# Performance work log

Hardware: AMD Instinct MI355X
Metric: run time of the kernel (lower is better)

## Reference

```python
import jax, jax.numpy as jnp
import numpy as np

B, NW, D, K = 16384, 32, 64, 512  # batch, n_windows, embedding_dim, codebook_size


def setup_inputs() -> dict:
    key = jax.random.key(0)
    k1, k2 = jax.random.split(key)
    ze = jax.random.normal(k1, (B, NW * D), dtype=jnp.float32)
    codebook = jax.random.normal(k2, (K, D), dtype=jnp.float32)
    return {"ze": ze, "codebook": codebook}


def reference(ze, codebook):
    # window-based VQ: split last dim into NW windows of size D, quantize each
    zew = ze.reshape(B, NW, D)
    # squared distances: ||ze||^2 + ||e||^2 - 2 ze.e^T  -> [B, NW, K]
    sq_norm = (
        jnp.sum(zew * zew, axis=-1, keepdims=True)
        + jnp.sum(codebook * codebook, axis=-1)
        - 2.0 * jnp.einsum("bwd,kd->bwk", zew, codebook)
    )
    indices = jnp.argmin(sq_norm, axis=-1)  # [B, NW]
    zq = codebook[indices].reshape(ze.shape)  # gather + concat over windows

    vq_e_loss = jnp.mean((zq - jax.lax.stop_gradient(ze)) ** 2)
    vq_commit_loss = jnp.mean((jax.lax.stop_gradient(zq) - ze) ** 2)

    # entropy term: counts of each code usage divided by 10 (as in original)
    counts = jnp.bincount(indices.reshape(-1), length=K)
    probs = counts.astype(jnp.float32) / 10.0
    entropy = jnp.sum(probs * jnp.log(probs + 1e-10))
    return indices, zq, vq_e_loss, vq_commit_loss, entropy
```

## Files before the change

### kernel.cpp

```cpp
#include <hip/hip_runtime.h>
#include <math.h>

#define DIM 64
#define KCB 512
#define NWIN 524288
#define ZQN (NWIN * DIM)
#define WPT 512
#define NBLK (NWIN / WPT)

typedef __attribute__((ext_vector_type(8))) short bf16x8;
typedef __attribute__((ext_vector_type(4))) float f32x4;

__device__ __forceinline__ unsigned bfbits(float f) { return __float_as_uint(f) >> 16; }

__device__ __forceinline__ int4 pack8(float4 a, float4 b) {
    int4 r;
    r.x = (int)(bfbits(a.x) | (__float_as_uint(a.y) & 0xffff0000u));
    r.y = (int)(bfbits(a.z) | (__float_as_uint(a.w) & 0xffff0000u));
    r.z = (int)(bfbits(b.x) | (__float_as_uint(b.y) & 0xffff0000u));
    r.w = (int)(bfbits(b.z) | (__float_as_uint(b.w) & 0xffff0000u));
    return r;
}

__global__ __launch_bounds__(512, 4) void vq_fused_kernel(
    const float* __restrict__ ze, const float* __restrict__ cb,
    float* __restrict__ out_idx, float* __restrict__ zq,
    int* __restrict__ counts, float* __restrict__ lossAcc)
{
    __shared__ int4  bfr[4096];
    __shared__ float norm_s[KCB];
    __shared__ int   hist_s[KCB];
    __shared__ int   idx_s[WPT];
    __shared__ float lpart[8];

    const int t    = threadIdx.x;
    const int lane = t & 63;
    const int wv   = t >> 6;
    const int q    = lane >> 4;
    const int l15  = lane & 15;
    const long blk = blockIdx.x;

    const float4* z4b = (const float4*)ze;

    float4 ld[16];
    {
        const float4* z4 = z4b + blk * (long)(WPT * 16);
        const int m = wv * 64 + l15;
#pragma unroll
        for (int tt = 0; tt < 4; ++tt)
#pragma unroll
            for (int h = 0; h < 2; ++h)
#pragma unroll
                for (int i = 0; i < 2; ++i)
                    ld[tt * 4 + h * 2 + i] = z4[(m + tt * 16) * 16 + h * 8 + q * 2 + i];
    }

    hist_s[t] = 0;

    {
        const float4* c4 = (const float4*)cb;
        float s = 0.f;
#pragma unroll
        for (int i = 0; i < 16; ++i) {
            float4 v = c4[t * 16 + i];
            s += v.x * v.x + v.y * v.y + v.z * v.z + v.w * v.w;
        }
        norm_s[t] = 0.5f * s;
    }

#pragma unroll
    for (int i = 0; i < 8; ++i) {
        int f = i * 512 + t;
        int L = f & 63, rest = f >> 6, h = rest & 1, c = rest >> 1;
        int n = c * 16 + (L & 15);
        int k = h * 32 + (L >> 4) * 8;
        const float4* s4 = (const float4*)(cb + n * DIM + k);
        bfr[(c * 2 + h) * 64 + L] = pack8(s4[0], s4[1]);
    }

    __syncthreads();

    bf16x8 afrag[4][2];
    float  znorm[4];
#pragma unroll
    for (int tt = 0; tt < 4; ++tt) {
        float part = 0.f;
#pragma unroll
        for (int h = 0; h < 2; ++h) {
            float4 a0 = ld[tt * 4 + h * 2], a1 = ld[tt * 4 + h * 2 + 1];
            part += a0.x*a0.x + a0.y*a0.y + a0.z*a0.z + a0.w*a0.w
                  + a1.x*a1.x + a1.y*a1.y + a1.z*a1.z + a1.w*a1.w;
            int4 p = pack8(a0, a1);
            p.x ^= 0x80008000; p.y ^= 0x80008000;
            p.z ^= 0x80008000; p.w ^= 0x80008000;
            afrag[tt][h] = __builtin_bit_cast(bf16x8, p);
        }
        part += __shfl_xor(part, 16, 64);
        part += __shfl_xor(part, 32, 64);
        znorm[tt] = part;
    }

    float best[4][4];
#pragma unroll
    for (int tt = 0; tt < 4; ++tt)
#pragma unroll
        for (int r = 0; r < 4; ++r) best[tt][r] = __uint_as_float(0x7e000000u);

    for (int cp = 0; cp < 16; ++cp) {
        f32x4 e0[4], e1[4];
        {
            const int c = 2 * cp;
            bf16x8 b0 = __builtin_bit_cast(bf16x8, bfr[(c * 2 + 0) * 64 + lane]);
            bf16x8 b1 = __builtin_bit_cast(bf16x8, bfr[(c * 2 + 1) * 64 + lane]);
            float nh = norm_s[c * 16 + l15];
            f32x4 nrm4 = {nh, nh, nh, nh};
#pragma unroll
            for (int tt = 0; tt < 4; ++tt) {
                e0[tt] = __builtin_amdgcn_mfma_f32_16x16x32_bf16(afrag[tt][0], b0, nrm4, 0, 0, 0);
                e0[tt] = __builtin_amdgcn_mfma_f32_16x16x32_bf16(afrag[tt][1], b1, e0[tt], 0, 0, 0);
            }
        }
        {
            const int c = 2 * cp + 1;
            bf16x8 b0 = __builtin_bit_cast(bf16x8, bfr[(c * 2 + 0) * 64 + lane]);
            bf16x8 b1 = __builtin_bit_cast(bf16x8, bfr[(c * 2 + 1) * 64 + lane]);
            float nh = norm_s[c * 16 + l15];
            f32x4 nrm4 = {nh, nh, nh, nh};
#pragma unroll
            for (int tt = 0; tt < 4; ++tt) {
                e1[tt] = __builtin_amdgcn_mfma_f32_16x16x32_bf16(afrag[tt][0], b0, nrm4, 0, 0, 0);
                e1[tt] = __builtin_amdgcn_mfma_f32_16x16x32_bf16(afrag[tt][1], b1, e1[tt], 0, 0, 0);
            }
        }
        const unsigned n0 = (unsigned)(2 * cp) * 16 + (unsigned)l15;
        const unsigned n1 = n0 + 16;
#pragma unroll
        for (int tt = 0; tt < 4; ++tt)
#pragma unroll
            for (int r = 0; r < 4; ++r) {
                float p0 = __uint_as_float((__float_as_uint(e0[tt][r]) & ~511u) | n0);
                float p1 = __uint_as_float((__float_as_uint(e1[tt][r]) & ~511u) | n1);
                best[tt][r] = fminf(fminf(best[tt][r], p0), p1);
            }
    }

#pragma unroll
    for (int tt = 0; tt < 4; ++tt)
#pragma unroll
        for (int r = 0; r < 4; ++r) {
            float v = best[tt][r];
            v = fminf(v, __shfl_xor(v, 1, 64));
            v = fminf(v, __shfl_xor(v, 2, 64));
            v = fminf(v, __shfl_xor(v, 4, 64));
            v = fminf(v, __shfl_xor(v, 8, 64));
            best[tt][r] = v;
        }

    float lsum = 0.f;
#pragma unroll
    for (int r = 0; r < 4; ++r) {
        if (l15 == q * 4 + r) {
#pragma unroll
            for (int tt = 0; tt < 4; ++tt) {
                unsigned bb = __float_as_uint(best[tt][r]);
                int   n  = (int)(bb & 511u);
                float sc = __uint_as_float(bb & ~511u);
                lsum += fmaf(2.f, sc, znorm[tt]);
                idx_s[wv * 64 + tt * 16 + l15] = n;
                atomicAdd(&hist_s[n], 1);
            }
        }
    }

    __syncthreads();

    out_idx[blk * (long)WPT + t] = (float)idx_s[t];

    {
        float4* zq4 = (float4*)zq;
        const long zb = blk * (long)(WPT * 16);
#pragma unroll
        for (int it = 0; it < 16; ++it) {
            int w_loc = it * 32 + (t >> 4);
            int j  = t & 15;
            int n  = idx_s[w_loc];
            int c  = n >> 4, ln = n & 15;
            int h  = j >> 3;
            int q2 = (j >> 1) & 3;
            int4 v = bfr[(c * 2 + h) * 64 + q2 * 16 + ln];
            int a  = (j & 1) ? v.z : v.x;
            int b  = (j & 1) ? v.w : v.y;
            float4 o;
            o.x = __uint_as_float((unsigned)a << 16);
            o.y = __uint_as_float((unsigned)a & 0xffff0000u);
            o.z = __uint_as_float((unsigned)b << 16);
            o.w = __uint_as_float((unsigned)b & 0xffff0000u);
            zq4[zb + (long)w_loc * 16 + j] = o;
        }
    }

#pragma unroll
    for (int off = 32; off; off >>= 1) lsum += __shfl_down(lsum, off, 64);
    if (lane == 0) lpart[wv] = lsum;
    __syncthreads();
    if (t == 0) {
        float s = 0.f;
#pragma unroll
        for (int i = 0; i < 8; ++i) s += lpart[i];
        atomicAdd(lossAcc, s);
    }
    {
        int h0 = hist_s[t];
        if (h0) atomicAdd(&counts[t], h0);
    }
}

__global__ __launch_bounds__(512) void vq_finalize_kernel(
    const int* __restrict__ counts, const float* __restrict__ lossAcc,
    float* __restrict__ outs)
{
    __shared__ float partial[8];
    const int t = threadIdx.x;

    float p = (float)counts[t] * 0.1f;
    float term = p * logf(p + 1e-10f);
#pragma unroll
    for (int off = 32; off; off >>= 1) term += __shfl_down(term, off, 64);
    if ((t & 63) == 0) partial[t >> 6] = term;
    __syncthreads();
    if (t == 0) {
        float e = 0.f;
#pragma unroll
        for (int i = 0; i < 8; ++i) e += partial[i];
        float loss = lossAcc[0] / (float)ZQN;
        outs[0] = loss;
        outs[1] = loss;
        outs[2] = e;
    }
}

extern "C" void kernel_launch(void* const* d_in, const int* in_sizes, int n_in,
                              void* d_out, int out_size, void* d_ws, size_t ws_size,
                              hipStream_t stream) {
    const float* ze = (const float*)d_in[0];
    const float* cb = (const float*)d_in[1];
    float* out = (float*)d_out;

    float* out_idx = out;
    float* out_zq  = out + NWIN;
    float* out_scl = out + NWIN + (long)ZQN;

    int*   counts  = (int*)d_ws;
    float* lossAcc = (float*)((char*)d_ws + KCB * sizeof(int));
    hipMemsetAsync(d_ws, 0, KCB * sizeof(int) + sizeof(float), stream);

    vq_fused_kernel<<<NBLK, 512, 0, stream>>>(ze, cb, out_idx, out_zq, counts, lossAcc);
    vq_finalize_kernel<<<1, KCB, 0, stream>>>(counts, lossAcc, out_scl);
}
```

Before: 269.5 us.

## Preformat codebook once in a separate kernel and stream B fragments from global

```diff
diff --git a/kernel.cpp b/kernel.cpp
--- a/kernel.cpp
+++ b/kernel.cpp
@@ -5,8 +5,8 @@
 #define KCB 512
 #define NWIN 524288
 #define ZQN (NWIN * DIM)
-#define WPT 512
-#define NBLK (NWIN / WPT)
+#define WPB 256
+#define NBLK (NWIN / WPB)
 
 typedef __attribute__((ext_vector_type(8))) short bf16x8;
 typedef __attribute__((ext_vector_type(4))) float f32x4;
@@ -22,16 +22,36 @@
     return r;
 }
 
-__global__ __launch_bounds__(512, 4) void vq_fused_kernel(
+__global__ __launch_bounds__(512) void vq_preformat_kernel(
+    const float* __restrict__ cb, int4* __restrict__ bfg, float* __restrict__ nrm)
+{
+    const int t = threadIdx.x;
+    const float4* c4 = (const float4*)cb;
+    float s = 0.f;
+#pragma unroll
+    for (int i = 0; i < 16; ++i) {
+        float4 v = c4[t * 16 + i];
+        s += v.x * v.x + v.y * v.y + v.z * v.z + v.w * v.w;
+    }
+    nrm[t] = 0.5f * s;
+#pragma unroll
+    for (int i = 0; i < 8; ++i) {
+        int f = i * 512 + t;
+        int L = f & 63, rest = f >> 6, h = rest & 1, c = rest >> 1;
+        int n = c * 16 + (L & 15);
+        int k = h * 32 + (L >> 4) * 8;
+        const float4* s4 = (const float4*)(cb + n * DIM + k);
+        bfg[(c * 2 + h) * 64 + L] = pack8(s4[0], s4[1]);
+    }
+}
+
+__global__ __launch_bounds__(256, 4) void vq_scan_kernel(
     const float* __restrict__ ze, const float* __restrict__ cb,
+    const int4* __restrict__ bfg, const float* __restrict__ nrm,
     float* __restrict__ out_idx, float* __restrict__ zq,
     int* __restrict__ counts, float* __restrict__ lossAcc)
 {
-    __shared__ int4  bfr[4096];
-    __shared__ float norm_s[KCB];
-    __shared__ int   hist_s[KCB];
-    __shared__ int   idx_s[WPT];
-    __shared__ float lpart[8];
+    __shared__ int idx_s[WPB];
 
     const int t    = threadIdx.x;
     const int lane = t & 63;
@@ -39,46 +59,19 @@
     const int q    = lane >> 4;
     const int l15  = lane & 15;
     const long blk = blockIdx.x;
-
-    const float4* z4b = (const float4*)ze;
-
-    float4 ld[16];
+    const long wbase = blk * (long)WPB + wv * 64;
+
+    float4 ldv[16];
     {
-        const float4* z4 = z4b + blk * (long)(WPT * 16);
-        const int m = wv * 64 + l15;
+        const float4* z4 = (const float4*)ze + wbase * 16;
 #pragma unroll
         for (int tt = 0; tt < 4; ++tt)
 #pragma unroll
             for (int h = 0; h < 2; ++h)
 #pragma unroll
                 for (int i = 0; i < 2; ++i)
-                    ld[tt * 4 + h * 2 + i] = z4[(m + tt * 16) * 16 + h * 8 + q * 2 + i];
-    }
-
-    hist_s[t] = 0;
-
-    {
-        const float4* c4 = (const float4*)cb;
-        float s = 0.f;
-#pragma unroll
-        for (int i = 0; i < 16; ++i) {
-            float4 v = c4[t * 16 + i];
-            s += v.x * v.x + v.y * v.y + v.z * v.z + v.w * v.w;
-        }
-        norm_s[t] = 0.5f * s;
-    }
-
-#pragma unroll
-    for (int i = 0; i < 8; ++i) {
-        int f = i * 512 + t;
-        int L = f & 63, rest = f >> 6, h = rest & 1, c = rest >> 1;
-        int n = c * 16 + (L & 15);
-        int k = h * 32 + (L >> 4) * 8;
-        const float4* s4 = (const float4*)(cb + n * DIM + k);
-        bfr[(c * 2 + h) * 64 + L] = pack8(s4[0], s4[1]);
-    }
-
-    __syncthreads();
+                    ldv[tt * 4 + h * 2 + i] = z4[(tt * 16 + l15) * 16 + h * 8 + q * 2 + i];
+    }
 
     bf16x8 afrag[4][2];
     float  znorm[4];
@@ -87,7 +80,7 @@
         float part = 0.f;
 #pragma unroll
         for (int h = 0; h < 2; ++h) {
-            float4 a0 = ld[tt * 4 + h * 2], a1 = ld[tt * 4 + h * 2 + 1];
+            float4 a0 = ldv[tt * 4 + h * 2], a1 = ldv[tt * 4 + h * 2 + 1];
             part += a0.x*a0.x + a0.y*a0.y + a0.z*a0.z + a0.w*a0.w
                   + a1.x*a1.x + a1.y*a1.y + a1.z*a1.z + a1.w*a1.w;
             int4 p = pack8(a0, a1);
@@ -106,33 +99,40 @@
 #pragma unroll
         for (int r = 0; r < 4; ++r) best[tt][r] = __uint_as_float(0x7e000000u);
 
+    bf16x8 pb0 = __builtin_bit_cast(bf16x8, bfg[0 * 64 + lane]);
+    bf16x8 pb1 = __builtin_bit_cast(bf16x8, bfg[1 * 64 + lane]);
+    bf16x8 pb2 = __builtin_bit_cast(bf16x8, bfg[2 * 64 + lane]);
+    bf16x8 pb3 = __builtin_bit_cast(bf16x8, bfg[3 * 64 + lane]);
+    float  pn0 = nrm[l15];
+    float  pn1 = nrm[16 + l15];
+
     for (int cp = 0; cp < 16; ++cp) {
         f32x4 e0[4], e1[4];
         {
-            const int c = 2 * cp;
-            bf16x8 b0 = __builtin_bit_cast(bf16x8, bfr[(c * 2 + 0) * 64 + lane]);
-            bf16x8 b1 = __builtin_bit_cast(bf16x8, bfr[(c * 2 + 1) * 64 + lane]);
-            float nh = norm_s[c * 16 + l15];
-            f32x4 nrm4 = {nh, nh, nh, nh};
+            f32x4 nrm4 = {pn0, pn0, pn0, pn0};
 #pragma unroll
             for (int tt = 0; tt < 4; ++tt) {
-                e0[tt] = __builtin_amdgcn_mfma_f32_16x16x32_bf16(afrag[tt][0], b0, nrm4, 0, 0, 0);
-                e0[tt] = __builtin_amdgcn_mfma_f32_16x16x32_bf16(afrag[tt][1], b1, e0[tt], 0, 0, 0);
+                e0[tt] = __builtin_amdgcn_mfma_f32_16x16x32_bf16(afrag[tt][0], pb0, nrm4, 0, 0, 0);
+                e0[tt] = __builtin_amdgcn_mfma_f32_16x16x32_bf16(afrag[tt][1], pb1, e0[tt], 0, 0, 0);
             }
         }
         {
-            const int c = 2 * cp + 1;
-            bf16x8 b0 = __builtin_bit_cast(bf16x8, bfr[(c * 2 + 0) * 64 + lane]);
-            bf16x8 b1 = __builtin_bit_cast(bf16x8, bfr[(c * 2 + 1) * 64 + lane]);
-            float nh = norm_s[c * 16 + l15];
-            f32x4 nrm4 = {nh, nh, nh, nh};
+            f32x4 nrm4 = {pn1, pn1, pn1, pn1};
 #pragma unroll
             for (int tt = 0; tt < 4; ++tt) {
-                e1[tt] = __builtin_amdgcn_mfma_f32_16x16x32_bf16(afrag[tt][0], b0, nrm4, 0, 0, 0);
-                e1[tt] = __builtin_amdgcn_mfma_f32_16x16x32_bf16(afrag[tt][1], b1, e1[tt], 0, 0, 0);
-            }
-        }
-        const unsigned n0 = (unsigned)(2 * cp) * 16 + (unsigned)l15;
+                e1[tt] = __builtin_amdgcn_mfma_f32_16x16x32_bf16(afrag[tt][0], pb2, nrm4, 0, 0, 0);
+                e1[tt] = __builtin_amdgcn_mfma_f32_16x16x32_bf16(afrag[tt][1], pb3, e1[tt], 0, 0, 0);
+            }
+        }
+        if (cp < 15) {
+            pb0 = __builtin_bit_cast(bf16x8, bfg[(4 * cp + 4) * 64 + lane]);
+            pb1 = __builtin_bit_cast(bf16x8, bfg[(4 * cp + 5) * 64 + lane]);
+            pb2 = __builtin_bit_cast(bf16x8, bfg[(4 * cp + 6) * 64 + lane]);
+            pb3 = __builtin_bit_cast(bf16x8, bfg[(4 * cp + 7) * 64 + lane]);
+            pn0 = nrm[(cp + 1) * 32 + l15];
+            pn1 = nrm[(cp + 1) * 32 + 16 + l15];
+        }
+        const unsigned n0 = (unsigned)cp * 32 + (unsigned)l15;
         const unsigned n1 = n0 + 16;
 #pragma unroll
         for (int tt = 0; tt < 4; ++tt)
@@ -167,52 +167,30 @@
                 float sc = __uint_as_float(bb & ~511u);
                 lsum += fmaf(2.f, sc, znorm[tt]);
                 idx_s[wv * 64 + tt * 16 + l15] = n;
-                atomicAdd(&hist_s[n], 1);
-            }
-        }
-    }
-
-    __syncthreads();
-
-    out_idx[blk * (long)WPT + t] = (float)idx_s[t];
+                atomicAdd(&counts[n], 1);
+            }
+        }
+    }
+    asm volatile("s_waitcnt lgkmcnt(0)" ::: "memory");
+
+    out_idx[wbase + lane] = (float)idx_s[wv * 64 + lane];
 
     {
-        float4* zq4 = (float4*)zq;
-        const long zb = blk * (long)(WPT * 16);
+        const f32x4* c4g = (const f32x4*)cb;
+        f32x4*       zq4 = (f32x4*)zq;
+        const long zb = wbase * 16;
 #pragma unroll
         for (int it = 0; it < 16; ++it) {
-            int w_loc = it * 32 + (t >> 4);
-            int j  = t & 15;
-            int n  = idx_s[w_loc];
-            int c  = n >> 4, ln = n & 15;
-            int h  = j >> 3;
-            int q2 = (j >> 1) & 3;
-            int4 v = bfr[(c * 2 + h) * 64 + q2 * 16 + ln];
-            int a  = (j & 1) ? v.z : v.x;
-            int b  = (j & 1) ? v.w : v.y;
-            float4 o;
-            o.x = __uint_as_float((unsigned)a << 16);
-            o.y = __uint_as_float((unsigned)a & 0xffff0000u);
-            o.z = __uint_as_float((unsigned)b << 16);
-            o.w = __uint_as_float((unsigned)b & 0xffff0000u);
-            zq4[zb + (long)w_loc * 16 + j] = o;
+            int w_loc = it * 4 + (lane >> 4);
+            int n = idx_s[wv * 64 + w_loc];
+            f32x4 o = c4g[n * 16 + l15];
+            zq4[zb + (long)w_loc * 16 + l15] = o;
         }
     }
 
 #pragma unroll
     for (int off = 32; off; off >>= 1) lsum += __shfl_down(lsum, off, 64);
-    if (lane == 0) lpart[wv] = lsum;
-    __syncthreads();
-    if (t == 0) {
-        float s = 0.f;
-#pragma unroll
-        for (int i = 0; i < 8; ++i) s += lpart[i];
-        atomicAdd(lossAcc, s);
-    }
-    {
-        int h0 = hist_s[t];
-        if (h0) atomicAdd(&counts[t], h0);
-    }
+    if (lane == 0) atomicAdd(lossAcc, lsum);
 }
 
 __global__ __launch_bounds__(512) void vq_finalize_kernel(
@@ -252,8 +230,12 @@
 
     int*   counts  = (int*)d_ws;
     float* lossAcc = (float*)((char*)d_ws + KCB * sizeof(int));
+    int4*  bfg     = (int4*)((char*)d_ws + 4096);
+    float* nrm     = (float*)((char*)d_ws + 4096 + 65536);
     hipMemsetAsync(d_ws, 0, KCB * sizeof(int) + sizeof(float), stream);
 
-    vq_fused_kernel<<<NBLK, 512, 0, stream>>>(ze, cb, out_idx, out_zq, counts, lossAcc);
+    vq_preformat_kernel<<<1, 512, 0, stream>>>(cb, bfg, nrm);
+    vq_scan_kernel<<<NBLK, 256, 0, stream>>>(ze, cb, bfg, nrm,
+                                             out_idx, out_zq, counts, lossAcc);
     vq_finalize_kernel<<<1, KCB, 0, stream>>>(counts, lossAcc, out_scl);
 }
```

Measured after the change: 709.4 us. +163.2%, slower.
